# Kernel tuning notes

Measured on AMD Instinct MI355X. Metric: run time of the kernel, lower is better.

Reference implementation:

```python
import jax, jax.numpy as jnp
from jax import lax
import numpy as np

R = 500          # Resampling: temporal segment width
H = 100          # fixed signal height from the reshape in forward
EPS = 1e-5       # BatchNorm2d default eps
FLAT = 6 * 31 * 32


def _cbrp(x, w, b, g, be, m, v):
    """Conv(5x5, pad 2) + inference BatchNorm + ReLU + MaxPool 2x2."""
    x = lax.conv_general_dilated(x, w, (1, 1), ((2, 2), (2, 2)),
                                 dimension_numbers=('NCHW', 'OIHW', 'NCHW'))
    x = x + b[None, :, None, None]
    inv = g * lax.rsqrt(v + EPS)
    x = x * inv[None, :, None, None] + (be - m * inv)[None, :, None, None]
    x = jax.nn.relu(x)
    return lax.reduce_window(x, -jnp.inf, lax.max, (1, 1, 2, 2), (1, 1, 2, 2), 'VALID')


def setup_inputs() -> dict:
    key = jax.random.key(0)
    ks = jax.random.split(key, 16)
    d = {}
    d['x'] = jax.random.normal(ks[0], (16, 1, 100, 4000), dtype=jnp.float32)
    chans = [(1, 16), (16, 32), (32, 64), (64, 32)]
    for i, (ci, co) in enumerate(chans, start=1):
        fan_in = ci * 25
        d[f'w{i}'] = jax.random.normal(ks[i], (co, ci, 5, 5), dtype=jnp.float32) * np.float32((2.0 / fan_in) ** 0.5)
        d[f'b{i}'] = jnp.zeros((co,), jnp.float32)
        d[f'g{i}'] = jnp.ones((co,), jnp.float32)
        d[f'be{i}'] = jnp.zeros((co,), jnp.float32)
        d[f'm{i}'] = jnp.zeros((co,), jnp.float32)
        d[f'v{i}'] = jnp.ones((co,), jnp.float32)
    d['fw1'] = jax.random.normal(ks[5], (32, FLAT), dtype=jnp.float32) * np.float32(FLAT ** -0.5)
    d['fb1'] = jnp.zeros((32,), jnp.float32)
    d['fw2'] = jax.random.normal(ks[6], (2, 32), dtype=jnp.float32) * np.float32(32 ** -0.5)
    d['fb2'] = jnp.zeros((2,), jnp.float32)
    return d


def reference(x, w1, b1, g1, be1, m1, v1,
              w2, b2, g2, be2, m2, v2,
              w3, b3, g3, be3, m3, v3,
              w4, b4, g4, be4, m4, v4,
              fw1, fb1, fw2, fb2):
    B = x.shape[0]
    L = x.shape[-1] // R  # number of temporal segments per sample
    # (B,1,100,L*R) -> (B*L,1,100,R): batch all segments into one conv call
    xs = x[:, 0].reshape(B, H, L, R).transpose(0, 2, 1, 3).reshape(B * L, 1, H, R)
    h = _cbrp(xs, w1, b1, g1, be1, m1, v1)   # (BL,16,50,250)
    h = _cbrp(h, w2, b2, g2, be2, m2, v2)    # (BL,32,25,125)
    h = _cbrp(h, w3, b3, g3, be3, m3, v3)    # (BL,64,12,62)
    h = _cbrp(h, w4, b4, g4, be4, m4, v4)    # (BL,32,6,31)
    h = h.reshape(B * L, FLAT)
    h = h @ fw1.T + fb1
    h = h @ fw2.T + fb2                      # (BL,2)
    return h.reshape(B, L, 2).mean(axis=1)   # average segment votes per sample
```

## Files before the change

kernel.cpp:

```cpp
#include <hip/hip_runtime.h>
#include <hip/hip_bf16.h>

#define EPSB 1e-5f

typedef short s16x8 __attribute__((ext_vector_type(8)));
typedef float f32x16 __attribute__((ext_vector_type(16)));

#define P1_OFF   0
#define P2_OFF   57507840
#define P3_OFF   89817088
#define PTOT     107642880
#define L4_OFF   107642880
#define H1_OFF   110690304
#define WT2_OFF  110706688
#define WT3_OFF  110732288
#define WT4_OFF  110834688
#define SS2_OFF  110937088
#define SS3_OFF  110937344
#define SS4_OFF  110937856

__device__ __forceinline__ unsigned short bf16bits(float f) {
    __hip_bfloat16 h = __float2bfloat16(f);
    union { __hip_bfloat16 h; unsigned short u; } cv; cv.h = h; return cv.u;
}

template<int HP, int WP, int C, int IH, int IW>
__global__ __launch_bounds__(256)
void pad_zero(__hip_bfloat16* __restrict__ buf)
{
    const int idx = blockIdx.x * 256 + threadIdx.x;
    if (idx >= 128 * HP * WP) return;
    const int rc = idx % (HP * WP);
    const int row = rc / WP, col = rc % WP;
    const bool pad = (row < 2) | (row >= 2 + IH) | (col < 2) | (col >= 2 + IW);
    if (!pad) return;
    int4* p = reinterpret_cast<int4*>(buf + (size_t)idx * C);
    #pragma unroll
    for (int i = 0; i < C * 2 / 16; ++i) p[i] = int4{0, 0, 0, 0};
}

__global__ __launch_bounds__(256)
void wtrans_kernel(const float* __restrict__ src, __hip_bfloat16* __restrict__ dst,
                   int CO, int CI)
{
    const int idx = blockIdx.x * 256 + threadIdx.x;
    if (idx >= CO * CI * 25) return;
    const int co  = idx / (CI * 25);
    const int rem = idx % (CI * 25);
    const int ci  = rem / 25;
    const int tap = rem % 25;
    dst[((size_t)tap * CO + co) * CI + ci] = __float2bfloat16(src[idx]);
}

__global__ __launch_bounds__(64)
void scsh_kernel(const float* __restrict__ b, const float* __restrict__ g,
                 const float* __restrict__ be, const float* __restrict__ m,
                 const float* __restrict__ v, float* __restrict__ out, int CO)
{
    const int i = threadIdx.x;
    if (i < CO) {
        const float sc = g[i] * rsqrtf(v[i] + EPSB);
        out[i]      = sc;
        out[CO + i] = fmaf(b[i] - m[i], sc, be[i]);
    }
}

__global__ __launch_bounds__(256)
void conv1_kernel(const float* __restrict__ x,
                  const float* __restrict__ wgt,
                  const float* __restrict__ bias,
                  const float* __restrict__ g,
                  const float* __restrict__ be,
                  const float* __restrict__ m,
                  const float* __restrict__ v,
                  __hip_bfloat16* __restrict__ p1)
{
    const int n   = blockIdx.y;
    const int idx = blockIdx.x * 256 + threadIdx.x;
    if (idx >= 50 * 250) return;
    const int ph = idx / 250, pw = idx % 250;

    const int b = n >> 3, l = n & 7;
    const float* ib = x + (size_t)b * 400000 + l * 500;

    const int h0  = 2 * ph - 2;
    const int w0c = 2 * pw - 2;
    float win[6][6];
    #pragma unroll
    for (int r = 0; r < 6; ++r) {
        const int hh = h0 + r;
        const bool vr = (hh >= 0) & (hh < 100);
        #pragma unroll
        for (int c = 0; c < 6; ++c) {
            const int ww = w0c + c;
            const bool ok = vr & (ww >= 0) & (ww < 500);
            win[r][c] = ok ? ib[hh * 4000 + ww] : 0.0f;
        }
    }

    float o[16];
    #pragma unroll
    for (int co = 0; co < 16; ++co) {
        float a0 = 0.f, a1 = 0.f, a2 = 0.f, a3 = 0.f;
        #pragma unroll
        for (int kh = 0; kh < 5; ++kh) {
            #pragma unroll
            for (int kw = 0; kw < 5; ++kw) {
                const float w = wgt[co * 25 + kh * 5 + kw];
                a0 = fmaf(w, win[kh  ][kw  ], a0);
                a1 = fmaf(w, win[kh  ][kw+1], a1);
                a2 = fmaf(w, win[kh+1][kw  ], a2);
                a3 = fmaf(w, win[kh+1][kw+1], a3);
            }
        }
        const float sc = g[co] * rsqrtf(v[co] + EPSB);
        const float sh = fmaf(bias[co] - m[co], sc, be[co]);
        #define RA(a) fmaxf(fmaf((a), sc, sh), 0.0f)
        o[co] = fmaxf(fmaxf(RA(a0), RA(a1)), fmaxf(RA(a2), RA(a3)));
        #undef RA
    }

    int4 v0, v1;
    v0.x = bf16bits(o[0])  | (bf16bits(o[1])  << 16);
    v0.y = bf16bits(o[2])  | (bf16bits(o[3])  << 16);
    v0.z = bf16bits(o[4])  | (bf16bits(o[5])  << 16);
    v0.w = bf16bits(o[6])  | (bf16bits(o[7])  << 16);
    v1.x = bf16bits(o[8])  | (bf16bits(o[9])  << 16);
    v1.y = bf16bits(o[10]) | (bf16bits(o[11]) << 16);
    v1.z = bf16bits(o[12]) | (bf16bits(o[13]) << 16);
    v1.w = bf16bits(o[14]) | (bf16bits(o[15]) << 16);
    int4* dst = reinterpret_cast<int4*>(
        p1 + (size_t)n * (54 * 260 * 16) + ((2 + ph) * 260 + (2 + pw)) * 16);
    dst[0] = v0;
    dst[1] = v1;
}

template<int CI, int CO, int HINP, int WINP, int HOUTP, int WOUTP,
         int PH, int PW, int NT, int NCOT, bool NCHW_OUT>
__global__ __launch_bounds__(256)
void conv_mfma(const __hip_bfloat16* __restrict__ pin,
               const __hip_bfloat16* __restrict__ wq,
               const float* __restrict__ scsh,
               void* __restrict__ pout)
{
    const int lane = threadIdx.x & 63;
    int t = blockIdx.x * 4 + (threadIdx.x >> 6);
    const int cot = t % NCOT; t /= NCOT;
    const int wt  = t % NT;   t /= NT;
    const int r   = t % PH;   t /= PH;
    const int n   = t;
    if (n >= 128) return;

    const int lw = lane & 31, loct = lane >> 5;
    const int co0 = cot * 32;
    const int w0  = wt * 32;

    const __hip_bfloat16* bbase = pin + (size_t)n * (HINP * WINP * CI)
                                + ((2 * r) * WINP + w0 + lw) * CI + loct * 8;
    const __hip_bfloat16* abase = wq + (co0 + lw) * CI + loct * 8;

    f32x16 acc0 = {};
    f32x16 acc1 = {};

    #pragma unroll
    for (int kw = 0; kw < 5; ++kw) {
        #pragma unroll
        for (int s = 0; s < CI / 16; ++s) {
            s16x8 bfr[6];
            #pragma unroll
            for (int j = 0; j < 6; ++j)
                bfr[j] = *reinterpret_cast<const s16x8*>(bbase + (j * WINP + kw) * CI + s * 16);
            #pragma unroll
            for (int kh = 0; kh < 5; ++kh) {
                const s16x8 a = *reinterpret_cast<const s16x8*>(
                    abase + (size_t)((kh * 5 + kw) * CO) * CI + s * 16);
                acc0 = __builtin_amdgcn_mfma_f32_32x32x16_bf16(a, bfr[kh],     acc0, 0, 0, 0);
                acc1 = __builtin_amdgcn_mfma_f32_32x32x16_bf16(a, bfr[kh + 1], acc1, 0, 0, 0);
            }
        }
    }

    const int pw = wt * 16 + (lw >> 1);
    const bool act = ((lane & 1) == 0) && (pw < PW);
    #pragma unroll
    for (int reg = 0; reg < 16; ++reg) {
        const int co = co0 + (reg & 3) + 8 * (reg >> 2) + 4 * loct;
        const float sc = scsh[co], sh = scsh[CO + co];
        const float v0 = fmaxf(fmaf(acc0[reg], sc, sh), 0.0f);
        const float v1 = fmaxf(fmaf(acc1[reg], sc, sh), 0.0f);
        float vm = fmaxf(v0, v1);
        vm = fmaxf(vm, __shfl_xor(vm, 1, 64));
        if (act) {
            if (NCHW_OUT) {
                ((float*)pout)[(((size_t)n * CO + co) * PH + r) * PW + pw] = vm;
            } else {
                ((__hip_bfloat16*)pout)[(size_t)n * (HOUTP * WOUTP * CO)
                    + ((2 + r) * WOUTP + (2 + pw)) * CO + co] = __float2bfloat16(vm);
            }
        }
    }
}

__global__ __launch_bounds__(64)
void fc1_kernel(const float* __restrict__ h,
                const float* __restrict__ fw1,
                const float* __restrict__ fb1,
                float* __restrict__ h1)
{
    const int n = blockIdx.x;
    const int j = blockIdx.y;
    const int lane = threadIdx.x;
    const float* hp = h   + (size_t)n * 5952;
    const float* wp = fw1 + (size_t)j * 5952;
    float s = 0.0f;
    for (int k = lane; k < 5952; k += 64) s = fmaf(hp[k], wp[k], s);
    #pragma unroll
    for (int off = 32; off > 0; off >>= 1) s += __shfl_down(s, off, 64);
    if (lane == 0) h1[n * 32 + j] = s + fb1[j];
}

__global__ __launch_bounds__(64)
void fc2_mean_kernel(const float* __restrict__ h1,
                     const float* __restrict__ fw2,
                     const float* __restrict__ fb2,
                     float* __restrict__ out)
{
    const int t = threadIdx.x;
    if (t >= 32) return;
    const int b = t >> 1, c = t & 1;
    float s = 0.0f;
    for (int l = 0; l < 8; ++l) {
        const float* hp = h1 + (size_t)(b * 8 + l) * 32;
        #pragma unroll
        for (int j = 0; j < 32; ++j) s = fmaf(hp[j], fw2[c * 32 + j], s);
    }
    out[t] = fmaf(s, 0.125f, fb2[c]);
}

extern "C" void kernel_launch(void* const* d_in, const int* in_sizes, int n_in,
                              void* d_out, int out_size, void* d_ws, size_t ws_size,
                              hipStream_t stream)
{
    const float* x   = (const float*)d_in[0];
    const float* w1  = (const float*)d_in[1];
    const float* b1  = (const float*)d_in[2];
    const float* g1  = (const float*)d_in[3];
    const float* be1 = (const float*)d_in[4];
    const float* m1  = (const float*)d_in[5];
    const float* v1  = (const float*)d_in[6];
    const float* w2  = (const float*)d_in[7];
    const float* b2  = (const float*)d_in[8];
    const float* g2  = (const float*)d_in[9];
    const float* be2 = (const float*)d_in[10];
    const float* m2  = (const float*)d_in[11];
    const float* v2  = (const float*)d_in[12];
    const float* w3  = (const float*)d_in[13];
    const float* b3  = (const float*)d_in[14];
    const float* g3  = (const float*)d_in[15];
    const float* be3 = (const float*)d_in[16];
    const float* m3  = (const float*)d_in[17];
    const float* v3  = (const float*)d_in[18];
    const float* w4  = (const float*)d_in[19];
    const float* b4  = (const float*)d_in[20];
    const float* g4  = (const float*)d_in[21];
    const float* be4 = (const float*)d_in[22];
    const float* m4  = (const float*)d_in[23];
    const float* v4  = (const float*)d_in[24];
    const float* fw1 = (const float*)d_in[25];
    const float* fb1 = (const float*)d_in[26];
    const float* fw2 = (const float*)d_in[27];
    const float* fb2 = (const float*)d_in[28];

    char* ws = (char*)d_ws;
    __hip_bfloat16* p1  = (__hip_bfloat16*)(ws + P1_OFF);
    __hip_bfloat16* p2  = (__hip_bfloat16*)(ws + P2_OFF);
    __hip_bfloat16* p3  = (__hip_bfloat16*)(ws + P3_OFF);
    float*          l4  = (float*)(ws + L4_OFF);
    float*          h1  = (float*)(ws + H1_OFF);
    __hip_bfloat16* wt2 = (__hip_bfloat16*)(ws + WT2_OFF);
    __hip_bfloat16* wt3 = (__hip_bfloat16*)(ws + WT3_OFF);
    __hip_bfloat16* wt4 = (__hip_bfloat16*)(ws + WT4_OFF);
    float*          ss2 = (float*)(ws + SS2_OFF);
    float*          ss3 = (float*)(ws + SS3_OFF);
    float*          ss4 = (float*)(ws + SS4_OFF);

    pad_zero<54, 260, 16, 50, 250><<<dim3(7020), 256, 0, stream>>>(p1);
    pad_zero<29, 136, 32, 25, 125><<<dim3(1858), 256, 0, stream>>>(p2);
    pad_zero<16,  68, 64, 12,  62><<<dim3(544),  256, 0, stream>>>(p3);

    wtrans_kernel<<<dim3(50),  256, 0, stream>>>(w2, wt2, 32, 16);
    wtrans_kernel<<<dim3(200), 256, 0, stream>>>(w3, wt3, 64, 32);
    wtrans_kernel<<<dim3(200), 256, 0, stream>>>(w4, wt4, 32, 64);
    scsh_kernel<<<1, 64, 0, stream>>>(b2, g2, be2, m2, v2, ss2, 32);
    scsh_kernel<<<1, 64, 0, stream>>>(b3, g3, be3, m3, v3, ss3, 64);
    scsh_kernel<<<1, 64, 0, stream>>>(b4, g4, be4, m4, v4, ss4, 32);

    conv1_kernel<<<dim3(49, 128), 256, 0, stream>>>(x, w1, b1, g1, be1, m1, v1, p1);

    conv_mfma<16, 32, 54, 260, 29, 136, 25, 125, 8, 1, false>
        <<<dim3(128 * 25 * 8 / 4), 256, 0, stream>>>(p1, wt2, ss2, p2);
    conv_mfma<32, 64, 29, 136, 16, 68, 12, 62, 4, 2, false>
        <<<dim3(128 * 12 * 4 * 2 / 4), 256, 0, stream>>>(p2, wt3, ss3, p3);
    conv_mfma<64, 32, 16, 68, 0, 0, 6, 31, 2, 1, true>
        <<<dim3(128 * 6 * 2 / 4), 256, 0, stream>>>(p3, wt4, ss4, l4);

    fc1_kernel<<<dim3(128, 32), 64, 0, stream>>>(l4, fw1, fb1, h1);
    fc2_mean_kernel<<<1, 64, 0, stream>>>(h1, fw2, fb2, (float*)d_out);
}
```

Measured before the change: 501.4 us.

## Compute two pooled rows per wave in MFMA convs; tune conv1 occupancy

Each wave in the MFMA conv kernels now computes RPW pooled output rows instead of one. Weight fragments are shared across 2*RPW accumulators, and the input rows that overlap between adjacent pooled rows are loaded once. This roughly halves the A-fragment loads and cuts redundant B loads for conv2 and conv3, at the cost of more accumulator registers and possibly lower occupancy. Conv1 gets a launch-bounds occupancy hint plus empty asm barriers that keep its input window in registers.

Result: faster. 470.7 us (-6.1%).

```diff
diff --git a/kernel.cpp b/kernel.cpp
--- a/kernel.cpp
+++ b/kernel.cpp
@@ -65,7 +65,7 @@
     }
 }
 
-__global__ __launch_bounds__(256)
+__global__ __launch_bounds__(256, 4)
 void conv1_kernel(const float* __restrict__ x,
                   const float* __restrict__ wgt,
                   const float* __restrict__ bias,
@@ -97,6 +97,11 @@
             win[r][c] = ok ? ib[hh * 4000 + ww] : 0.0f;
         }
     }
+    #pragma unroll
+    for (int r = 0; r < 6; ++r)
+        #pragma unroll
+        for (int c = 0; c < 6; ++c)
+            asm volatile("" : "+v"(win[r][c]));
 
     float o[16];
     #pragma unroll
@@ -136,18 +141,20 @@
 }
 
 template<int CI, int CO, int HINP, int WINP, int HOUTP, int WOUTP,
-         int PH, int PW, int NT, int NCOT, bool NCHW_OUT>
+         int PH, int PW, int NT, int NCOT, int RPW, bool NCHW_OUT>
 __global__ __launch_bounds__(256)
 void conv_mfma(const __hip_bfloat16* __restrict__ pin,
                const __hip_bfloat16* __restrict__ wq,
                const float* __restrict__ scsh,
                void* __restrict__ pout)
 {
+    constexpr int R = (PH + RPW - 1) / RPW;
+    constexpr int NROW = 2 * RPW + 4;
     const int lane = threadIdx.x & 63;
     int t = blockIdx.x * 4 + (threadIdx.x >> 6);
     const int cot = t % NCOT; t /= NCOT;
     const int wt  = t % NT;   t /= NT;
-    const int r   = t % PH;   t /= PH;
+    const int r   = t % R;    t /= R;
     const int n   = t;
     if (n >= 128) return;
 
@@ -156,26 +163,30 @@
     const int w0  = wt * 32;
 
     const __hip_bfloat16* bbase = pin + (size_t)n * (HINP * WINP * CI)
-                                + ((2 * r) * WINP + w0 + lw) * CI + loct * 8;
+                                + (w0 + lw) * CI + loct * 8;
     const __hip_bfloat16* abase = wq + (co0 + lw) * CI + loct * 8;
 
-    f32x16 acc0 = {};
-    f32x16 acc1 = {};
+    f32x16 acc[2 * RPW];
+    #pragma unroll
+    for (int q = 0; q < 2 * RPW; ++q) acc[q] = (f32x16){};
 
     #pragma unroll
     for (int kw = 0; kw < 5; ++kw) {
         #pragma unroll
         for (int s = 0; s < CI / 16; ++s) {
-            s16x8 bfr[6];
+            s16x8 bfr[NROW];
             #pragma unroll
-            for (int j = 0; j < 6; ++j)
-                bfr[j] = *reinterpret_cast<const s16x8*>(bbase + (j * WINP + kw) * CI + s * 16);
+            for (int j = 0; j < NROW; ++j) {
+                const int row = (2 * RPW * r + j < HINP) ? (2 * RPW * r + j) : (HINP - 1);
+                bfr[j] = *reinterpret_cast<const s16x8*>(bbase + (row * WINP + kw) * CI + s * 16);
+            }
             #pragma unroll
             for (int kh = 0; kh < 5; ++kh) {
                 const s16x8 a = *reinterpret_cast<const s16x8*>(
                     abase + (size_t)((kh * 5 + kw) * CO) * CI + s * 16);
-                acc0 = __builtin_amdgcn_mfma_f32_32x32x16_bf16(a, bfr[kh],     acc0, 0, 0, 0);
-                acc1 = __builtin_amdgcn_mfma_f32_32x32x16_bf16(a, bfr[kh + 1], acc1, 0, 0, 0);
+                #pragma unroll
+                for (int q = 0; q < 2 * RPW; ++q)
+                    acc[q] = __builtin_amdgcn_mfma_f32_32x32x16_bf16(a, bfr[kh + q], acc[q], 0, 0, 0);
             }
         }
     }
@@ -183,19 +194,24 @@
     const int pw = wt * 16 + (lw >> 1);
     const bool act = ((lane & 1) == 0) && (pw < PW);
     #pragma unroll
-    for (int reg = 0; reg < 16; ++reg) {
-        const int co = co0 + (reg & 3) + 8 * (reg >> 2) + 4 * loct;
-        const float sc = scsh[co], sh = scsh[CO + co];
-        const float v0 = fmaxf(fmaf(acc0[reg], sc, sh), 0.0f);
-        const float v1 = fmaxf(fmaf(acc1[reg], sc, sh), 0.0f);
-        float vm = fmaxf(v0, v1);
-        vm = fmaxf(vm, __shfl_xor(vm, 1, 64));
-        if (act) {
-            if (NCHW_OUT) {
-                ((float*)pout)[(((size_t)n * CO + co) * PH + r) * PW + pw] = vm;
-            } else {
-                ((__hip_bfloat16*)pout)[(size_t)n * (HOUTP * WOUTP * CO)
-                    + ((2 + r) * WOUTP + (2 + pw)) * CO + co] = __float2bfloat16(vm);
+    for (int p = 0; p < RPW; ++p) {
+        const int pr = RPW * r + p;
+        const bool rok = (pr < PH);
+        #pragma unroll
+        for (int reg = 0; reg < 16; ++reg) {
+            const int co = co0 + (reg & 3) + 8 * (reg >> 2) + 4 * loct;
+            const float sc = scsh[co], sh = scsh[CO + co];
+            const float v0 = fmaxf(fmaf(acc[2 * p    ][reg], sc, sh), 0.0f);
+            const float v1 = fmaxf(fmaf(acc[2 * p + 1][reg], sc, sh), 0.0f);
+            float vm = fmaxf(v0, v1);
+            vm = fmaxf(vm, __shfl_xor(vm, 1, 64));
+            if (act && rok) {
+                if (NCHW_OUT) {
+                    ((float*)pout)[(((size_t)n * CO + co) * PH + pr) * PW + pw] = vm;
+                } else {
+                    ((__hip_bfloat16*)pout)[(size_t)n * (HOUTP * WOUTP * CO)
+                        + ((2 + pr) * WOUTP + (2 + pw)) * CO + co] = __float2bfloat16(vm);
+                }
             }
         }
     }
@@ -297,11 +313,11 @@
 
     conv1_kernel<<<dim3(49, 128), 256, 0, stream>>>(x, w1, b1, g1, be1, m1, v1, p1);
 
-    conv_mfma<16, 32, 54, 260, 29, 136, 25, 125, 8, 1, false>
-        <<<dim3(128 * 25 * 8 / 4), 256, 0, stream>>>(p1, wt2, ss2, p2);
-    conv_mfma<32, 64, 29, 136, 16, 68, 12, 62, 4, 2, false>
-        <<<dim3(128 * 12 * 4 * 2 / 4), 256, 0, stream>>>(p2, wt3, ss3, p3);
-    conv_mfma<64, 32, 16, 68, 0, 0, 6, 31, 2, 1, true>
+    conv_mfma<16, 32, 54, 260, 29, 136, 25, 125, 8, 1, 2, false>
+        <<<dim3(128 * 13 * 8 / 4), 256, 0, stream>>>(p1, wt2, ss2, p2);
+    conv_mfma<32, 64, 29, 136, 16, 68, 12, 62, 4, 2, 2, false>
+        <<<dim3(128 * 6 * 4 * 2 / 4), 256, 0, stream>>>(p2, wt3, ss3, p3);
+    conv_mfma<64, 32, 16, 68, 0, 0, 6, 31, 2, 1, 1, true>
         <<<dim3(128 * 6 * 2 / 4), 256, 0, stream>>>(p3, wt4, ss4, l4);
 
     fc1_kernel<<<dim3(128, 32), 64, 0, stream>>>(l4, fw1, fb1, h1);
```
